# Kernel tuning notes

Hardware: AMD Instinct MI355X
Metric: run time of the kernel (lower is better)

The kernel has to match this reference:

```python
import jax, jax.numpy as jnp
import numpy as np
import math

D_MODEL = 1024
N_HEADS = 16
D_K = D_MODEL // N_HEADS
D_FF = 4096
B, S = 2, 1024
EPS = 1e-6
MASK_FILL = 1e-9  # source uses masked_fill_(mask==0, 1e-09), NOT -inf


def layer_norm(x, alpha, bias):
    # torch: mean + unbiased std (ddof=1), normalized by (std + eps)
    mean = jnp.mean(x, axis=-1, keepdims=True)
    std = jnp.std(x, axis=-1, keepdims=True, ddof=1)
    return alpha * (x - mean) / (std + EPS) + bias


def setup_inputs() -> dict:
    key = jax.random.key(0)
    ks = jax.random.split(key, 6)
    sc = 0.02
    return {
        "x": jax.random.normal(ks[0], (B, S, D_MODEL), jnp.float32),
        "mask": jax.random.randint(ks[1], (B, 1, S, S), 0, 2, jnp.int32),
        "Wq": jax.random.normal(ks[2], (D_MODEL, D_MODEL), jnp.float32) * sc,
        "Wo": jax.random.normal(ks[3], (D_MODEL, D_MODEL), jnp.float32) * sc,
        "W1": jax.random.normal(ks[4], (D_MODEL, D_FF), jnp.float32) * sc,
        "B1": jnp.zeros((D_FF,), jnp.float32),
        "W2": jax.random.normal(ks[5], (D_FF, D_MODEL), jnp.float32) * sc,
        "B2": jnp.zeros((D_MODEL,), jnp.float32),
        "ln1_a": jnp.ones((D_MODEL,), jnp.float32),
        "ln1_b": jnp.zeros((D_MODEL,), jnp.float32),
        "ln2_a": jnp.ones((D_MODEL,), jnp.float32),
        "ln2_b": jnp.zeros((D_MODEL,), jnp.float32),
    }


def reference(x, mask, Wq, Wo, W1, B1, W2, B2, ln1_a, ln1_b, ln2_a, ln2_b):
    # --- residual 1: pre-norm self-attention ---
    n = layer_norm(x, ln1_a, ln1_b)
    # source bug preserved: Wq is applied to q, k AND v; q==k==v here
    qkv = (n @ Wq).reshape(B, S, N_HEADS, D_K).transpose(0, 2, 1, 3)  # [B,H,S,dk]
    scores = jnp.einsum('bhqd,bhkd->bhqk', qkv, qkv) / math.sqrt(D_K)
    scores = jnp.where(mask == 0, MASK_FILL, scores)
    attn = jax.nn.softmax(scores, axis=-1)
    ctx = jnp.einsum('bhqk,bhkd->bhqd', attn, qkv)
    ctx = ctx.transpose(0, 2, 1, 3).reshape(B, S, D_MODEL)
    x = x + ctx @ Wo
    # --- residual 2: pre-norm FFN ---
    n2 = layer_norm(x, ln2_a, ln2_b)
    ff = jax.nn.relu(n2 @ W1 + B1) @ W2 + B2
    return x + ff
```

## Files before the change

kernel.cpp:

```cpp
#include <hip/hip_runtime.h>
#include <hip/hip_bf16.h>
#include <stdint.h>

#define D_MODEL 1024
#define S_LEN 1024
#define BATCH 2
#define NHEADS 16
#define DK 64
#define DFF 4096

typedef __attribute__((ext_vector_type(8))) short short8;
typedef __attribute__((ext_vector_type(4))) float f32x4;

__device__ __forceinline__ unsigned short f2bf(float f) {
  union { float f; unsigned u; } v; v.f = f;
  unsigned r = v.u + 0x7FFFu + ((v.u >> 16) & 1u);
  return (unsigned short)(r >> 16);
}

__device__ __forceinline__ float bf2f(unsigned short s) {
  union { float f; unsigned u; } v; v.u = ((unsigned)s) << 16;
  return v.f;
}

__device__ __forceinline__ void gll16(const void* g, void* l) {
  __builtin_amdgcn_global_load_lds(
      (const __attribute__((address_space(1))) void*)g,
      (__attribute__((address_space(3))) void*)l, 16, 0, 0);
}

__global__ __launch_bounds__(256)
void ln_kernel(const float* __restrict__ x,
               const float* __restrict__ alpha,
               const float* __restrict__ beta,
               unsigned short* __restrict__ out) {
  const int row = blockIdx.x;
  const int tid = threadIdx.x;
  const float4 v = ((const float4*)(x + (int64_t)row * D_MODEL))[tid];
  float s = v.x + v.y + v.z + v.w;
  float ss = v.x * v.x + v.y * v.y + v.z * v.z + v.w * v.w;
  #pragma unroll
  for (int m = 32; m; m >>= 1) {
    s += __shfl_down(s, m);
    ss += __shfl_down(ss, m);
  }
  __shared__ float red[10];
  const int wave = tid >> 6;
  if ((tid & 63) == 0) { red[wave] = s; red[4 + wave] = ss; }
  __syncthreads();
  if (tid == 0) {
    float S = red[0] + red[1] + red[2] + red[3];
    float SS = red[4] + red[5] + red[6] + red[7];
    float mean = S * (1.f / 1024.f);
    float var = (SS - 1024.f * mean * mean) * (1.f / 1023.f);
    float inv = 1.f / (sqrtf(fmaxf(var, 0.f)) + 1e-6f);
    red[8] = mean; red[9] = inv;
  }
  __syncthreads();
  const float mean = red[8], inv = red[9];
  const float4 a = ((const float4*)alpha)[tid];
  const float4 bb = ((const float4*)beta)[tid];
  union { unsigned short us[4]; uint2 u2; } pk;
  pk.us[0] = f2bf(a.x * (v.x - mean) * inv + bb.x);
  pk.us[1] = f2bf(a.y * (v.y - mean) * inv + bb.y);
  pk.us[2] = f2bf(a.z * (v.z - mean) * inv + bb.z);
  pk.us[3] = f2bf(a.w * (v.w - mean) * inv + bb.w);
  ((uint2*)(out + (int64_t)row * D_MODEL))[tid] = pk.u2;
}

__global__ __launch_bounds__(256)
void wtall_kernel(const float* __restrict__ Wq, const float* __restrict__ Wo,
                  const float* __restrict__ W1, const float* __restrict__ W2,
                  unsigned short* __restrict__ WqT, unsigned short* __restrict__ WoT,
                  unsigned short* __restrict__ W1T, unsigned short* __restrict__ W2T) {
  __shared__ unsigned short tile[32][33];
  int id = blockIdx.x;
  const float* W; unsigned short* Wt; int K, N, bx, by;
  if (id < 1024)      { W = Wq; Wt = WqT; K = 1024; N = 1024; bx = id & 31;  by = id >> 5; }
  else if (id < 2048) { id -= 1024; W = Wo; Wt = WoT; K = 1024; N = 1024; bx = id & 31;  by = id >> 5; }
  else if (id < 6144) { id -= 2048; W = W1; Wt = W1T; K = 1024; N = 4096; bx = id & 127; by = id >> 7; }
  else                { id -= 6144; W = W2; Wt = W2T; K = 4096; N = 1024; bx = id & 31;  by = id >> 5; }
  const int k0 = by * 32, n0 = bx * 32;
  const int tx = threadIdx.x & 31, ty = threadIdx.x >> 5;
  #pragma unroll
  for (int i = 0; i < 4; i++) {
    int r = ty + i * 8;
    tile[r][tx] = f2bf(W[(int64_t)(k0 + r) * N + n0 + tx]);
  }
  __syncthreads();
  #pragma unroll
  for (int i = 0; i < 4; i++) {
    int r = ty + i * 8;
    Wt[(int64_t)(n0 + r) * K + k0 + tx] = tile[tx][r];
  }
}

__global__ __launch_bounds__(256)
void qkvt_kernel(const unsigned short* __restrict__ qkv,
                 unsigned short* __restrict__ qkvT) {
  __shared__ unsigned short tile[32][33];
  const int s0 = blockIdx.x * 32, d0 = blockIdx.y * 32, bh = blockIdx.z;
  const int b = bh >> 4, h = bh & 15;
  const int tx = threadIdx.x & 31, ty = threadIdx.x >> 5;
  #pragma unroll
  for (int i = 0; i < 4; i++) {
    int r = ty + i * 8;
    tile[r][tx] = qkv[(int64_t)(b * S_LEN + s0 + r) * D_MODEL + h * DK + d0 + tx];
  }
  __syncthreads();
  #pragma unroll
  for (int i = 0; i < 4; i++) {
    int r = ty + i * 8;
    qkvT[(int64_t)(bh * DK + d0 + r) * S_LEN + s0 + tx] = tile[tx][r];
  }
}

__global__ __launch_bounds__(256)
void mprep_kernel(const int* __restrict__ mask, unsigned short* __restrict__ Mf) {
  const int gid = blockIdx.x * 256 + threadIdx.x;
  const int lo = gid & 15;
  const int ktb = (gid >> 4) & 31;
  const int q4 = (gid >> 9) & 255;
  const int b = gid >> 17;
  const int* mrow = mask + ((int64_t)b << 20) + (int64_t)q4 * 4096 + ktb * 32 + lo;
  union { unsigned short us[8]; short8 v; } o;
  #pragma unroll
  for (int r = 0; r < 4; r++) {
    o.us[r * 2]     = mrow[r * 1024]      ? 0x3F80 : 0;
    o.us[r * 2 + 1] = mrow[r * 1024 + 16] ? 0x3F80 : 0;
  }
  ((short8*)Mf)[gid] = o.v;
}

template<int BM, int BN, int BK, int BIAS, int RELU, int RES, int OUTBF, int KSPLIT>
__global__ __launch_bounds__(256)
void gemm_t(const unsigned short* __restrict__ A,
            const unsigned short* __restrict__ Bt,
            const float* __restrict__ bias,
            const float* __restrict__ res,
            void* __restrict__ outp,
            void* __restrict__ outp2,
            int M, int N, int K) {
  constexpr int NCH = BK / 8;
  constexpr int RPW = 512 / BK;
  constexpr int RPR = 2048 / BK;
  constexpr int RA = (BM * BK) / 2048;
  constexpr int RB = (BN * BK) / 2048;
  constexpr int MI = BM / 32;
  constexpr int NJ = BN / 32;
  constexpr int KK = BK / 32;

  __shared__ __align__(16) unsigned short As[BM * BK];
  __shared__ __align__(16) unsigned short Bs[BN * BK];

  const int tid = threadIdx.x;
  const int lane = tid & 63;
  const int wave = tid >> 6;
  const int lo = lane & 15, hi = lane >> 4;

  int bid = blockIdx.x;
  int split = 0;
  if (KSPLIT == 2) { split = bid & 1; bid >>= 1; }
  const int cpx = (gridDim.x / KSPLIT) >> 3;
  const int sid = (bid & 7) * cpx + (bid >> 3);
  const int nbx = N / BN;
  const int n0 = (sid % nbx) * BN;
  const int m0 = (sid / nbx) * BM;
  const int wr = (wave >> 1) * (BM / 2);
  const int wc = (wave & 1) * (BN / 2);

  auto swz = [](int row, int c) -> int {
    if (BK == 128) return c ^ ((row & 7) << 1);
    if (BK == 64)  return c ^ (row & 7);
    return c ^ ((row >> 1) & 3);
  };

  const int sr = lane / NCH;
  const int sc = lane % NCH;

  f32x4 acc[MI][NJ] = {};

  const int kbeg = split * (K / KSPLIT);
  const int kend = kbeg + K / KSPLIT;
  for (int k0 = kbeg; k0 < kend; k0 += BK) {
    #pragma unroll
    for (int r = 0; r < RA; r++) {
      const int row = r * RPR + wave * RPW + sr;
      gll16(A + (int64_t)(m0 + row) * K + k0 + swz(row, sc) * 8,
            &As[r * 2048 + wave * 512]);
    }
    #pragma unroll
    for (int r = 0; r < RB; r++) {
      const int row = r * RPR + wave * RPW + sr;
      gll16(Bt + (int64_t)(n0 + row) * K + k0 + swz(row, sc) * 8,
            &Bs[r * 2048 + wave * 512]);
    }
    __syncthreads();
    #pragma unroll
    for (int kk = 0; kk < KK; kk++) {
      short8 af[MI], bfr[NJ];
      #pragma unroll
      for (int t = 0; t < MI; t++) {
        const int row = wr + t * 16 + lo;
        af[t] = *(const short8*)&As[row * BK + swz(row, kk * 4 + hi) * 8];
      }
      #pragma unroll
      for (int t = 0; t < NJ; t++) {
        const int row = wc + t * 16 + lo;
        bfr[t] = *(const short8*)&Bs[row * BK + swz(row, kk * 4 + hi) * 8];
      }
      #pragma unroll
      for (int i = 0; i < MI; i++)
        #pragma unroll
        for (int j = 0; j < NJ; j++)
          acc[i][j] = __builtin_amdgcn_mfma_f32_16x16x32_bf16(af[i], bfr[j], acc[i][j], 0, 0, 0);
    }
    __syncthreads();
  }

  float* Pout = (KSPLIT == 2) ? (split ? (float*)outp2 : (float*)outp) : nullptr;
  #pragma unroll
  for (int i = 0; i < MI; i++) {
    const int row = m0 + wr + i * 16 + hi * 4;
    #pragma unroll
    for (int j = 0; j < NJ; j++) {
      const int col = n0 + wc + j * 16 + lo;
      #pragma unroll
      for (int r = 0; r < 4; r++) {
        float v = acc[i][j][r];
        if (KSPLIT == 2) {
          Pout[(int64_t)(row + r) * N + col] = v;
        } else {
          if (BIAS) v += bias[col];
          if (RELU) v = fmaxf(v, 0.f);
          if (RES)  v += res[(int64_t)(row + r) * N + col];
          if (OUTBF)
            ((unsigned short*)outp)[(int64_t)(row + r) * N + col] = f2bf(v);
          else
            ((float*)outp)[(int64_t)(row + r) * N + col] = v;
        }
      }
    }
  }
}

__global__ __launch_bounds__(256)
void fcomb_kernel(const float* __restrict__ P0, const float* __restrict__ P1,
                  const float* __restrict__ bias, float* __restrict__ out) {
  const int i4 = blockIdx.x * 256 + threadIdx.x;
  const float4 a = ((const float4*)P0)[i4];
  const float4 b = ((const float4*)P1)[i4];
  const float4 bb = ((const float4*)bias)[i4 & 255];
  float4 c = ((const float4*)out)[i4];
  c.x += a.x + b.x + bb.x;
  c.y += a.y + b.y + bb.y;
  c.z += a.z + b.z + bb.z;
  c.w += a.w + b.w + bb.w;
  ((float4*)out)[i4] = c;
}

__global__ __launch_bounds__(256)
void attn_kernel(const unsigned short* __restrict__ qkv,
                 const unsigned short* __restrict__ qkvT,
                 const unsigned short* __restrict__ Mf,
                 float* __restrict__ part,
                 float* __restrict__ psum) {
  __shared__ __align__(16) unsigned short Ks[64 * 64];
  __shared__ __align__(16) unsigned short Vs[64 * 64];
  __shared__ __align__(16) unsigned short Ms[512 * 8];
  __shared__ __align__(16) unsigned short Plds[4][16 * 40];
  const int tid = threadIdx.x;
  const int lane = tid & 63;
  const int wave = tid >> 6;
  const int lo = lane & 15, hi = lane >> 4;
  const int L = blockIdx.x;
  const int xcd = L & 7, idx = L >> 3;
  const int b = xcd >> 2;
  const int h = (xcd & 3) * 4 + (idx >> 5);
  const int split = (idx >> 4) & 1;
  const int qt = idx & 15;
  const int bh = b * 16 + h;
  const int q0 = qt * 64 + wave * 16;

  const unsigned short* qb =
      qkv + (int64_t)(b * S_LEN + q0 + lo) * D_MODEL + h * DK + hi * 8;
  const short8 qf0 = *(const short8*)qb;
  const short8 qf1 = *(const short8*)(qb + 32);

  f32x4 oacc[4] = {};
  float rsum[4] = {0.f, 0.f, 0.f, 0.f};
  unsigned short* Pw = Plds[wave];
  const int kbeg = split * 512;
  const int q4w = wave * 4 + hi;
  const int xr = lo & 7;

  for (int kti = 0; kti < 8; kti++) {
    const int kt = kbeg + kti * 64;
    #pragma unroll
    for (int r = 0; r < 2; r++) {
      const int c = r * 256 + tid;
      const int row = c >> 3;
      const int chg = (c & 7) ^ (row & 7);
      gll16(qkv + (int64_t)(b * S_LEN + kt + row) * D_MODEL + h * DK + chg * 8,
            &Ks[(r * 256 + wave * 64) * 8]);
      gll16(qkvT + (int64_t)(bh * DK + row) * S_LEN + kt + chg * 8,
            &Vs[(r * 256 + wave * 64) * 8]);
      const int q4l = c >> 5;
      const int u2 = (c >> 4) & 1;
      const int log = (c & 15) ^ q4l;
      gll16(Mf + ((int64_t)((b * 256 + qt * 16 + q4l) * 32 + (kt >> 5) + u2) * 16 + log) * 8,
            &Ms[(r * 256 + wave * 64) * 8]);
    }
    __syncthreads();
    #pragma unroll
    for (int u = 0; u < 2; u++) {
      const short8 kf00 = *(const short8*)&Ks[((u * 32 + lo) * 8 + (hi ^ xr)) * 8];
      const short8 kf01 = *(const short8*)&Ks[((u * 32 + lo) * 8 + ((4 + hi) ^ xr)) * 8];
      const short8 kf10 = *(const short8*)&Ks[((u * 32 + 16 + lo) * 8 + (hi ^ xr)) * 8];
      const short8 kf11 = *(const short8*)&Ks[((u * 32 + 16 + lo) * 8 + ((4 + hi) ^ xr)) * 8];
      const short8 mf = *(const short8*)&Ms[(q4w * 32 + u * 16 + (lo ^ q4w)) * 8];
      f32x4 s0 = {}, s1 = {};
      s0 = __builtin_amdgcn_mfma_f32_16x16x32_bf16(qf0, kf00, s0, 0, 0, 0);
      s0 = __builtin_amdgcn_mfma_f32_16x16x32_bf16(qf1, kf01, s0, 0, 0, 0);
      s1 = __builtin_amdgcn_mfma_f32_16x16x32_bf16(qf0, kf10, s1, 0, 0, 0);
      s1 = __builtin_amdgcn_mfma_f32_16x16x32_bf16(qf1, kf11, s1, 0, 0, 0);
      #pragma unroll
      for (int r = 0; r < 4; r++) {
        const float m0_ = bf2f((unsigned short)mf[r * 2]);
        const float m1_ = bf2f((unsigned short)mf[r * 2 + 1]);
        const float e0_ = __expf(s0[r] * 0.125f);
        const float e1_ = __expf(s1[r] * 0.125f);
        const float p0_ = fmaf(m0_, e0_ - 1.f, 1.f);
        const float p1_ = fmaf(m1_, e1_ - 1.f, 1.f);
        rsum[r] += p0_ + p1_;
        Pw[(hi * 4 + r) * 40 + lo]      = f2bf(p0_);
        Pw[(hi * 4 + r) * 40 + 16 + lo] = f2bf(p1_);
      }
      const short8 pf = *(const short8*)&Pw[lo * 40 + hi * 8];
      #pragma unroll
      for (int t = 0; t < 4; t++) {
        const short8 vf = *(const short8*)&Vs[((t * 16 + lo) * 8 + ((u * 4 + hi) ^ xr)) * 8];
        oacc[t] = __builtin_amdgcn_mfma_f32_16x16x32_bf16(pf, vf, oacc[t], 0, 0, 0);
      }
    }
    __syncthreads();
  }

  #pragma unroll
  for (int m = 1; m < 16; m <<= 1)
    #pragma unroll
    for (int r = 0; r < 4; r++) rsum[r] += __shfl_xor(rsum[r], m);

  const int64_t prow = (int64_t)(split * 32 + bh) * 1024;
  #pragma unroll
  for (int t = 0; t < 4; t++)
    #pragma unroll
    for (int r = 0; r < 4; r++)
      part[(prow + q0 + hi * 4 + r) * 64 + t * 16 + lo] = oacc[t][r];
  if (lo == 0)
    #pragma unroll
    for (int r = 0; r < 4; r++)
      psum[prow + q0 + hi * 4 + r] = rsum[r];
}

__global__ __launch_bounds__(256)
void acomb_kernel(const float* __restrict__ part,
                  const float* __restrict__ psum,
                  unsigned short* __restrict__ ctx) {
  const int idx4 = blockIdx.x * 256 + threadIdx.x;
  const int d4 = idx4 & 15;
  const int q = (idx4 >> 4) & 1023;
  const int bh = idx4 >> 14;
  const int b = bh >> 4, h = bh & 15;
  const float4* p4 = (const float4*)part;
  const float4 a0 = p4[(int64_t)(bh * 1024 + q) * 16 + d4];
  const float4 a1 = p4[524288 + (int64_t)(bh * 1024 + q) * 16 + d4];
  const float rs = psum[bh * 1024 + q] + psum[32768 + bh * 1024 + q];
  const float inv = 1.f / rs;
  union { unsigned short us[4]; uint2 u2; } pk;
  pk.us[0] = f2bf((a0.x + a1.x) * inv);
  pk.us[1] = f2bf((a0.y + a1.y) * inv);
  pk.us[2] = f2bf((a0.z + a1.z) * inv);
  pk.us[3] = f2bf((a0.w + a1.w) * inv);
  *(uint2*)(ctx + (int64_t)(b * S_LEN + q) * D_MODEL + h * DK + d4 * 4) = pk.u2;
}

extern "C" void kernel_launch(void* const* d_in, const int* in_sizes, int n_in,
                              void* d_out, int out_size, void* d_ws, size_t ws_size,
                              hipStream_t stream) {
  (void)in_sizes; (void)n_in; (void)out_size; (void)ws_size;
  const float* x    = (const float*)d_in[0];
  const int*   mask = (const int*)d_in[1];
  const float* Wq   = (const float*)d_in[2];
  const float* Wo   = (const float*)d_in[3];
  const float* W1   = (const float*)d_in[4];
  const float* B1   = (const float*)d_in[5];
  const float* W2   = (const float*)d_in[6];
  const float* B2   = (const float*)d_in[7];
  const float* ln1a = (const float*)d_in[8];
  const float* ln1b = (const float*)d_in[9];
  const float* ln2a = (const float*)d_in[10];
  const float* ln2b = (const float*)d_in[11];
  float* out = (float*)d_out;

  char* ws = (char*)d_ws;
  unsigned short* WqT  = (unsigned short*)(ws);
  unsigned short* WoT  = (unsigned short*)(ws + (2ull  << 20));
  unsigned short* W1T  = (unsigned short*)(ws + (4ull  << 20));
  float*          Pf0  = (float*)(ws + (4ull  << 20));
  unsigned short* W2T  = (unsigned short*)(ws + (12ull << 20));
  unsigned short* n1   = (unsigned short*)(ws + (20ull << 20));
  float*          psum = (float*)(ws + (20ull << 20));
  unsigned short* qkv  = (unsigned short*)(ws + (24ull << 20));
  unsigned short* qkvT = (unsigned short*)(ws + (28ull << 20));
  unsigned short* Mf   = (unsigned short*)(ws + (32ull << 20));
  unsigned short* ctx  = (unsigned short*)(ws + (32ull << 20));
  float*          Pf1  = (float*)(ws + (32ull << 20));
  unsigned short* n2   = (unsigned short*)(ws + (36ull << 20));
  float*          part = (float*)(ws + (40ull << 20));
  unsigned short* h1   = (unsigned short*)(ws + (40ull << 20));
  float* x1 = out;

  dim3 blk(256);
  wtall_kernel<<<10240, blk, 0, stream>>>(Wq, Wo, W1, W2, WqT, WoT, W1T, W2T);
  mprep_kernel<<<1024, blk, 0, stream>>>(mask, Mf);

  ln_kernel<<<2048, blk, 0, stream>>>(x, ln1a, ln1b, n1);
  gemm_t<64,64,128, 0,0,0,1,1><<<512, blk, 0, stream>>>(n1, WqT, nullptr, nullptr, qkv, nullptr, 2048, 1024, 1024);
  qkvt_kernel<<<dim3(32, 2, 32), blk, 0, stream>>>(qkv, qkvT);
  attn_kernel<<<1024, blk, 0, stream>>>(qkv, qkvT, Mf, part, psum);
  acomb_kernel<<<2048, blk, 0, stream>>>(part, psum, ctx);
  gemm_t<64,64,128, 0,0,1,0,1><<<512, blk, 0, stream>>>(ctx, WoT, nullptr, x, x1, nullptr, 2048, 1024, 1024);
  ln_kernel<<<2048, blk, 0, stream>>>(x1, ln2a, ln2b, n2);
  gemm_t<64,128,64, 1,1,0,1,1><<<1024, blk, 0, stream>>>(n2, W1T, B1, nullptr, h1, nullptr, 2048, 4096, 1024);
  gemm_t<64,64,128, 0,0,0,0,2><<<1024, blk, 0, stream>>>(h1, W2T, nullptr, nullptr, Pf0, Pf1, 2048, 1024, 4096);
  fcomb_kernel<<<2048, blk, 0, stream>>>(Pf0, Pf1, B2, out);
}
```

Before: 139.1 us.

## Fuse prep kernels into one launch and add intra-block split-K GEMM

Combines the weight transpose/convert, mask preprocessing and first LayerNorm into a single prep kernel dispatched by block index, which cuts the launch count. Adds a new 64x64 GEMM in which each of the four waves computes the full output tile over a different quarter of each 128-wide K chunk, then reduces the partial sums through LDS. This replaces the old tiled GEMM for the Q, O and W2 projections. The design trades extra LDS reduction traffic and single-buffered loads for simpler wave work and possibly better MFMA utilisation.

```diff
diff --git a/kernel.cpp b/kernel.cpp
--- a/kernel.cpp
+++ b/kernel.cpp
@@ -27,6 +27,86 @@
   __builtin_amdgcn_global_load_lds(
       (const __attribute__((address_space(1))) void*)g,
       (__attribute__((address_space(3))) void*)l, 16, 0, 0);
+}
+
+__global__ __launch_bounds__(256)
+void prep_kernel(const float* __restrict__ Wq, const float* __restrict__ Wo,
+                 const float* __restrict__ W1, const float* __restrict__ W2,
+                 const float* __restrict__ x, const float* __restrict__ ln1a,
+                 const float* __restrict__ ln1b, const int* __restrict__ mask,
+                 unsigned short* __restrict__ WqT, unsigned short* __restrict__ WoT,
+                 unsigned short* __restrict__ W1T, unsigned short* __restrict__ W2T,
+                 unsigned short* __restrict__ Mf, unsigned short* __restrict__ n1) {
+  __shared__ unsigned short tile[32][33];
+  __shared__ float red[10];
+  const int id = blockIdx.x;
+  const int tid = threadIdx.x;
+  if (id < 10240) {
+    int wid = id;
+    const float* W; unsigned short* Wt; int K, N, bx, by;
+    if (wid < 1024)      { W = Wq; Wt = WqT; K = 1024; N = 1024; bx = wid & 31;  by = wid >> 5; }
+    else if (wid < 2048) { wid -= 1024; W = Wo; Wt = WoT; K = 1024; N = 1024; bx = wid & 31;  by = wid >> 5; }
+    else if (wid < 6144) { wid -= 2048; W = W1; Wt = W1T; K = 1024; N = 4096; bx = wid & 127; by = wid >> 7; }
+    else                 { wid -= 6144; W = W2; Wt = W2T; K = 4096; N = 1024; bx = wid & 31;  by = wid >> 5; }
+    const int k0 = by * 32, n0 = bx * 32;
+    const int tx = tid & 31, ty = tid >> 5;
+    #pragma unroll
+    for (int i = 0; i < 4; i++) {
+      int r = ty + i * 8;
+      tile[r][tx] = f2bf(W[(int64_t)(k0 + r) * N + n0 + tx]);
+    }
+    __syncthreads();
+    #pragma unroll
+    for (int i = 0; i < 4; i++) {
+      int r = ty + i * 8;
+      Wt[(int64_t)(n0 + r) * K + k0 + tx] = tile[tx][r];
+    }
+  } else if (id < 11264) {
+    const int gid = (id - 10240) * 256 + tid;
+    const int lo = gid & 15;
+    const int ktb = (gid >> 4) & 31;
+    const int q4 = (gid >> 9) & 255;
+    const int b = gid >> 17;
+    const int* mrow = mask + ((int64_t)b << 20) + (int64_t)q4 * 4096 + ktb * 32 + lo;
+    union { unsigned short us[8]; short8 v; } o;
+    #pragma unroll
+    for (int r = 0; r < 4; r++) {
+      o.us[r * 2]     = mrow[r * 1024]      ? 0x3F80 : 0;
+      o.us[r * 2 + 1] = mrow[r * 1024 + 16] ? 0x3F80 : 0;
+    }
+    ((short8*)Mf)[gid] = o.v;
+  } else {
+    const int row = id - 11264;
+    const float4 v = ((const float4*)(x + (int64_t)row * D_MODEL))[tid];
+    float s = v.x + v.y + v.z + v.w;
+    float ss = v.x * v.x + v.y * v.y + v.z * v.z + v.w * v.w;
+    #pragma unroll
+    for (int m = 32; m; m >>= 1) {
+      s += __shfl_down(s, m);
+      ss += __shfl_down(ss, m);
+    }
+    const int wave = tid >> 6;
+    if ((tid & 63) == 0) { red[wave] = s; red[4 + wave] = ss; }
+    __syncthreads();
+    if (tid == 0) {
+      float S = red[0] + red[1] + red[2] + red[3];
+      float SS = red[4] + red[5] + red[6] + red[7];
+      float mean = S * (1.f / 1024.f);
+      float var = (SS - 1024.f * mean * mean) * (1.f / 1023.f);
+      float inv = 1.f / (sqrtf(fmaxf(var, 0.f)) + 1e-6f);
+      red[8] = mean; red[9] = inv;
+    }
+    __syncthreads();
+    const float mean = red[8], inv = red[9];
+    const float4 a = ((const float4*)ln1a)[tid];
+    const float4 bb = ((const float4*)ln1b)[tid];
+    union { unsigned short us[4]; uint2 u2; } pk;
+    pk.us[0] = f2bf(a.x * (v.x - mean) * inv + bb.x);
+    pk.us[1] = f2bf(a.y * (v.y - mean) * inv + bb.y);
+    pk.us[2] = f2bf(a.z * (v.z - mean) * inv + bb.z);
+    pk.us[3] = f2bf(a.w * (v.w - mean) * inv + bb.w);
+    ((uint2*)(n1 + (int64_t)row * D_MODEL))[tid] = pk.u2;
+  }
 }
 
 __global__ __launch_bounds__(256)
@@ -69,33 +149,6 @@
 }
 
 __global__ __launch_bounds__(256)
-void wtall_kernel(const float* __restrict__ Wq, const float* __restrict__ Wo,
-                  const float* __restrict__ W1, const float* __restrict__ W2,
-                  unsigned short* __restrict__ WqT, unsigned short* __restrict__ WoT,
-                  unsigned short* __restrict__ W1T, unsigned short* __restrict__ W2T) {
-  __shared__ unsigned short tile[32][33];
-  int id = blockIdx.x;
-  const float* W; unsigned short* Wt; int K, N, bx, by;
-  if (id < 1024)      { W = Wq; Wt = WqT; K = 1024; N = 1024; bx = id & 31;  by = id >> 5; }
-  else if (id < 2048) { id -= 1024; W = Wo; Wt = WoT; K = 1024; N = 1024; bx = id & 31;  by = id >> 5; }
-  else if (id < 6144) { id -= 2048; W = W1; Wt = W1T; K = 1024; N = 4096; bx = id & 127; by = id >> 7; }
-  else                { id -= 6144; W = W2; Wt = W2T; K = 4096; N = 1024; bx = id & 31;  by = id >> 5; }
-  const int k0 = by * 32, n0 = bx * 32;
-  const int tx = threadIdx.x & 31, ty = threadIdx.x >> 5;
-  #pragma unroll
-  for (int i = 0; i < 4; i++) {
-    int r = ty + i * 8;
-    tile[r][tx] = f2bf(W[(int64_t)(k0 + r) * N + n0 + tx]);
-  }
-  __syncthreads();
-  #pragma unroll
-  for (int i = 0; i < 4; i++) {
-    int r = ty + i * 8;
-    Wt[(int64_t)(n0 + r) * K + k0 + tx] = tile[tx][r];
-  }
-}
-
-__global__ __launch_bounds__(256)
 void qkvt_kernel(const unsigned short* __restrict__ qkv,
                  unsigned short* __restrict__ qkvT) {
   __shared__ unsigned short tile[32][33];
@@ -115,21 +168,131 @@
   }
 }
 
-__global__ __launch_bounds__(256)
-void mprep_kernel(const int* __restrict__ mask, unsigned short* __restrict__ Mf) {
-  const int gid = blockIdx.x * 256 + threadIdx.x;
-  const int lo = gid & 15;
-  const int ktb = (gid >> 4) & 31;
-  const int q4 = (gid >> 9) & 255;
-  const int b = gid >> 17;
-  const int* mrow = mask + ((int64_t)b << 20) + (int64_t)q4 * 4096 + ktb * 32 + lo;
-  union { unsigned short us[8]; short8 v; } o;
-  #pragma unroll
-  for (int r = 0; r < 4; r++) {
-    o.us[r * 2]     = mrow[r * 1024]      ? 0x3F80 : 0;
-    o.us[r * 2 + 1] = mrow[r * 1024 + 16] ? 0x3F80 : 0;
-  }
-  ((short8*)Mf)[gid] = o.v;
+template<int BIAS, int RELU, int RES, int OUTBF, int KSPLIT>
+__global__ __launch_bounds__(256)
+void gemm_wk(const unsigned short* __restrict__ A,
+             const unsigned short* __restrict__ Bt,
+             const float* __restrict__ bias,
+             const float* __restrict__ res,
+             void* __restrict__ outp,
+             void* __restrict__ outp2,
+             int M, int N, int K) {
+  constexpr int BK = 128;
+  __shared__ __align__(16) unsigned short S[2][8192];
+
+  const int tid = threadIdx.x;
+  const int lane = tid & 63;
+  const int wave = tid >> 6;
+  const int lo = lane & 15, hi = lane >> 4;
+
+  int bid = blockIdx.x;
+  int split = 0;
+  if (KSPLIT == 2) { split = bid & 1; bid >>= 1; }
+  const int cpx = (gridDim.x / KSPLIT) >> 3;
+  const int sid = (bid & 7) * cpx + (bid >> 3);
+  const int nbx = N >> 6;
+  const int n0 = (sid % nbx) << 6;
+  const int m0 = (sid / nbx) << 6;
+
+  auto swz = [](int row, int c) -> int { return c ^ ((row & 7) << 1); };
+
+  const int sr = lane >> 4;
+  const int sc = lane & 15;
+
+  f32x4 acc[4][4] = {};
+
+  const int kbeg = split * (K / KSPLIT);
+  const int kend = kbeg + K / KSPLIT;
+  const int ch = wave * 4 + hi;
+
+  for (int k0 = kbeg; k0 < kend; k0 += BK) {
+    #pragma unroll
+    for (int r = 0; r < 4; r++) {
+      const int row = r * 16 + wave * 4 + sr;
+      gll16(A + (int64_t)(m0 + row) * K + k0 + swz(row, sc) * 8,
+            &S[0][r * 2048 + wave * 512]);
+      gll16(Bt + (int64_t)(n0 + row) * K + k0 + swz(row, sc) * 8,
+            &S[1][r * 2048 + wave * 512]);
+    }
+    __syncthreads();
+    short8 af[4], bf[4];
+    #pragma unroll
+    for (int t = 0; t < 4; t++) {
+      const int row = t * 16 + lo;
+      af[t] = *(const short8*)&S[0][row * BK + swz(row, ch) * 8];
+      bf[t] = *(const short8*)&S[1][row * BK + swz(row, ch) * 8];
+    }
+    #pragma unroll
+    for (int i = 0; i < 4; i++)
+      #pragma unroll
+      for (int j = 0; j < 4; j++)
+        acc[i][j] = __builtin_amdgcn_mfma_f32_16x16x32_bf16(af[i], bf[j], acc[i][j], 0, 0, 0);
+    __syncthreads();
+  }
+
+  float* red = (float*)&S[0][0];
+  if (wave >= 2) {
+    #pragma unroll
+    for (int i = 0; i < 4; i++)
+      #pragma unroll
+      for (int j = 0; j < 4; j++)
+        *(f32x4*)&red[(wave - 2) * 4096 + (i * 4 + j) * 256 + lane * 4] = acc[i][j];
+  }
+  __syncthreads();
+  if (wave < 2) {
+    #pragma unroll
+    for (int i = 0; i < 4; i++)
+      #pragma unroll
+      for (int j = 0; j < 4; j++)
+        acc[i][j] += *(const f32x4*)&red[wave * 4096 + (i * 4 + j) * 256 + lane * 4];
+  }
+  __syncthreads();
+  if (wave == 1) {
+    #pragma unroll
+    for (int i = 0; i < 4; i++)
+      #pragma unroll
+      for (int jj = 0; jj < 2; jj++)
+        *(f32x4*)&red[(i * 2 + jj) * 256 + lane * 4] = acc[i][jj];
+  } else if (wave == 0) {
+    #pragma unroll
+    for (int i = 0; i < 4; i++)
+      #pragma unroll
+      for (int jj = 0; jj < 2; jj++)
+        *(f32x4*)&red[2048 + (i * 2 + jj) * 256 + lane * 4] = acc[i][2 + jj];
+  }
+  __syncthreads();
+
+  if (wave < 2) {
+    const int jb = wave * 2;
+    const int base = wave ? 2048 : 0;
+    float* Pout = (KSPLIT == 2) ? (split ? (float*)outp2 : (float*)outp) : nullptr;
+    #pragma unroll
+    for (int i = 0; i < 4; i++) {
+      const int row = m0 + i * 16 + hi * 4;
+      #pragma unroll
+      for (int jj = 0; jj < 2; jj++) {
+        const int j = jb + jj;
+        f32x4 v4 = acc[i][j];
+        v4 += *(const f32x4*)&red[base + (i * 2 + jj) * 256 + lane * 4];
+        const int col = n0 + j * 16 + lo;
+        #pragma unroll
+        for (int r = 0; r < 4; r++) {
+          float v = v4[r];
+          if (KSPLIT == 2) {
+            Pout[(int64_t)(row + r) * N + col] = v;
+          } else {
+            if (BIAS) v += bias[col];
+            if (RELU) v = fmaxf(v, 0.f);
+            if (RES)  v += res[(int64_t)(row + r) * N + col];
+            if (OUTBF)
+              ((unsigned short*)outp)[(int64_t)(row + r) * N + col] = f2bf(v);
+            else
+              ((float*)outp)[(int64_t)(row + r) * N + col] = v;
+          }
+        }
+      }
+    }
+  }
 }
 
 template<int BM, int BN, int BK, int BIAS, int RELU, int RES, int OUTBF, int KSPLIT>
@@ -422,17 +585,15 @@
   float* x1 = out;
 
   dim3 blk(256);
-  wtall_kernel<<<10240, blk, 0, stream>>>(Wq, Wo, W1, W2, WqT, WoT, W1T, W2T);
-  mprep_kernel<<<1024, blk, 0, stream>>>(mask, Mf);
-
-  ln_kernel<<<2048, blk, 0, stream>>>(x, ln1a, ln1b, n1);
-  gemm_t<64,64,128, 0,0,0,1,1><<<512, blk, 0, stream>>>(n1, WqT, nullptr, nullptr, qkv, nullptr, 2048, 1024, 1024);
+  prep_kernel<<<13312, blk, 0, stream>>>(Wq, Wo, W1, W2, x, ln1a, ln1b, mask,
+                                         WqT, WoT, W1T, W2T, Mf, n1);
+  gemm_wk<0,0,0,1,1><<<512, blk, 0, stream>>>(n1, WqT, nullptr, nullptr, qkv, nullptr, 2048, 1024, 1024);
   qkvt_kernel<<<dim3(32, 2, 32), blk, 0, stream>>>(qkv, qkvT);
   attn_kernel<<<1024, blk, 0, stream>>>(qkv, qkvT, Mf, part, psum);
   acomb_kernel<<<2048, blk, 0, stream>>>(part, psum, ctx);
-  gemm_t<64,64,128, 0,0,1,0,1><<<512, blk, 0, stream>>>(ctx, WoT, nullptr, x, x1, nullptr, 2048, 1024, 1024);
+  gemm_wk<0,0,1,0,1><<<512, blk, 0, stream>>>(ctx, WoT, nullptr, x, x1, nullptr, 2048, 1024, 1024);
   ln_kernel<<<2048, blk, 0, stream>>>(x1, ln2a, ln2b, n2);
   gemm_t<64,128,64, 1,1,0,1,1><<<1024, blk, 0, stream>>>(n2, W1T, B1, nullptr, h1, nullptr, 2048, 4096, 1024);
-  gemm_t<64,64,128, 0,0,0,0,2><<<1024, blk, 0, stream>>>(h1, W2T, nullptr, nullptr, Pf0, Pf1, 2048, 1024, 4096);
+  gemm_wk<0,0,0,0,2><<<1024, blk, 0, stream>>>(h1, W2T, nullptr, nullptr, Pf0, Pf1, 2048, 1024, 4096);
   fcomb_kernel<<<2048, blk, 0, stream>>>(Pf0, Pf1, B2, out);
 }
```

New measurement: 518.2 us. +272.6%, slower.
